# Kernel optimization log

Hardware: AMD Instinct MI355X
Metric: run time of the kernel (lower is better)

## Reference

```python
import jax, jax.numpy as jnp
import numpy as np


def setup_inputs() -> dict:
    key = jax.random.key(0)
    k1, k2, k3 = jax.random.split(key, 3)
    B, T, D = 32, 1024, 512
    x = jax.random.normal(k1, (B, T, D), dtype=jnp.float32)
    duration = jax.random.randint(k2, (B, T), 0, 9, dtype=jnp.int32)
    mask = jax.random.randint(k3, (B, T), 0, 2, dtype=jnp.int32)
    max_len = 2600  # static upper bound on max_b sum_t duration[b,t]
    return {"x": x, "duration": duration, "mask": mask, "max_len": max_len}


def reference(x, duration, mask, max_len):
    # x: [B, T, D]; duration, mask: [B, T]; max_len: python int (static)
    B, T, D = x.shape
    d_eff = duration * mask                       # masked tokens contribute 0 frames
    cum = jnp.cumsum(d_eff, axis=1)               # [B, T] cumulative frame counts
    total = cum[:, -1:]                           # [B, 1] frames per sequence
    pos = jnp.arange(max_len, dtype=cum.dtype)    # [T_out]
    # token index owning output frame j: #{t : cum[t] <= j}
    idx = jax.vmap(lambda c: jnp.searchsorted(c, pos, side='right'))(cum)  # [B, T_out]
    idx = jnp.minimum(idx, T - 1)
    valid = (pos[None, :] < total).astype(x.dtype)                         # [B, T_out]
    expanded = jnp.take_along_axis(x, idx[..., None], axis=1) * valid[..., None]
    return expanded, valid
```

## Files before the change

### kernel.cpp

```cpp
#include <hip/hip_runtime.h>

__global__ void lr_scan_kernel(const int* __restrict__ duration,
                               const int* __restrict__ mask,
                               int* __restrict__ cum, int T) {
    const int b = blockIdx.x;
    const int t = threadIdx.x;
    const int lane = t & 63;
    const int wave = t >> 6;
    __shared__ int wsum[4];

    const int4 dv = ((const int4*)(duration + (size_t)b * T))[t];
    const int4 mv = ((const int4*)(mask     + (size_t)b * T))[t];
    const int e0 = dv.x * mv.x, e1 = dv.y * mv.y,
              e2 = dv.z * mv.z, e3 = dv.w * mv.w;
    const int s3 = e0 + e1 + e2 + e3;

    int s = s3;
    #pragma unroll
    for (int off = 1; off < 64; off <<= 1) {
        int u = __shfl_up(s, off, 64);
        if (lane >= off) s += u;
    }
    if (lane == 63) wsum[wave] = s;
    __syncthreads();
    int bof = 0;
    #pragma unroll
    for (int w = 0; w < 4; ++w) bof += (w < wave) ? wsum[w] : 0;
    const int excl = bof + s - s3;

    int4 o;
    o.x = excl + e0;
    o.y = o.x + e1;
    o.z = o.y + e2;
    o.w = o.z + e3;
    ((int4*)(cum + (size_t)b * T))[t] = o;
}

__global__ __launch_bounds__(256)
void lr_fill_kernel(const int* __restrict__ cum,
                    int* __restrict__ idx,
                    float* __restrict__ valid_out,
                    int T, int max_len, int nwork) {
    const int gid = blockIdx.x * 256 + threadIdx.x;
    if (gid >= nwork) return;
    const unsigned b = (unsigned)gid / (unsigned)max_len;
    const int p = gid - (int)(b * (unsigned)max_len);

    const int* __restrict__ c = cum + (size_t)b * T;
    const int total = c[T - 1];
    if (p < total) {
        int lo = 0, hi = T;
        while (lo < hi) {
            int mid = (lo + hi) >> 1;
            if (c[mid] <= p) lo = mid + 1; else hi = mid;
        }
        idx[gid] = (lo < T - 1) ? lo : (T - 1);
        valid_out[gid] = 1.0f;
    } else {
        idx[gid] = -1;
        valid_out[gid] = 0.0f;
    }
}

__global__ __launch_bounds__(256)
void lr_copy_kernel(const float* __restrict__ x,
                    const int* __restrict__ idx,
                    float* __restrict__ out,
                    int T, int max_len, int nblk) {
    const int cpx = nblk >> 3;
    const int bid = blockIdx.x;
    const int swz = (bid & 7) * cpx + (bid >> 3);

    const int wave = threadIdx.x >> 6;
    const int lane = threadIdx.x & 63;
    const unsigned pos0 = (unsigned)swz * 8u + (unsigned)wave * 2u;
    const unsigned pos1 = pos0 + 1u;
    const unsigned b0 = pos0 / (unsigned)max_len;
    const unsigned b1 = pos1 / (unsigned)max_len;

    const int i0 = idx[pos0];
    const int i1 = idx[pos1];

    const float4 z = make_float4(0.f, 0.f, 0.f, 0.f);
    float4 a0 = z, a1 = z, c0 = z, c1 = z;
    if (i0 >= 0) {
        const float4* __restrict__ s0 =
            (const float4*)(x + ((size_t)b0 * T + i0) * 512u);
        a0 = s0[lane]; a1 = s0[lane + 64];
    }
    if (i1 >= 0) {
        const float4* __restrict__ s1 =
            (const float4*)(x + ((size_t)b1 * T + i1) * 512u);
        c0 = s1[lane]; c1 = s1[lane + 64];
    }
    float4* __restrict__ d0 = (float4*)(out + (size_t)pos0 * 512u);
    float4* __restrict__ d1 = (float4*)(out + (size_t)pos1 * 512u);
    d0[lane] = a0; d0[lane + 64] = a1;
    d1[lane] = c0; d1[lane + 64] = c1;
}

extern "C" void kernel_launch(void* const* d_in, const int* in_sizes, int n_in,
                              void* d_out, int out_size, void* d_ws, size_t ws_size,
                              hipStream_t stream) {
    const float* x        = (const float*)d_in[0];
    const int*   duration = (const int*)d_in[1];
    const int*   mask     = (const int*)d_in[2];

    const int B = 32;
    const int BT = in_sizes[1];
    const int T = BT / B;
    const int D = in_sizes[0] / BT;
    const int max_len = out_size / (B * (D + 1));

    float* out       = (float*)d_out;
    float* valid_out = out + (size_t)B * max_len * D;
    int*   cum       = (int*)d_ws;
    int*   idx       = cum + (size_t)B * T;

    lr_scan_kernel<<<B, 256, 0, stream>>>(duration, mask, cum, T);

    const int nwork = B * max_len;
    lr_fill_kernel<<<(nwork + 255) / 256, 256, 0, stream>>>(
        cum, idx, valid_out, T, max_len, nwork);

    const int nblk = nwork / 8;
    lr_copy_kernel<<<nblk, 256, 0, stream>>>(x, idx, out, T, max_len, nblk);
}
```

Baseline: 42.37 us.

## Fuse searchsorted into copy kernel with branchless search and nontemporal stores

Removes the separate fill kernel and the idx workspace. The copy kernel now does its own binary search over the cumulative counts, unrolled and branchless with power-of-two steps, and also writes the valid flags. Output stores become nontemporal. This saves a kernel launch and the idx round trip through memory. In exchange every wave repeats the search, and the fixed 512-step search assumes T is 1024.

New measurement: 42.67 us. No clear change (+0.7%).

```diff
diff --git a/kernel.cpp b/kernel.cpp
--- a/kernel.cpp
+++ b/kernel.cpp
@@ -1,4 +1,7 @@
 #include <hip/hip_runtime.h>
+
+typedef float f32x4 __attribute__((ext_vector_type(4)));
+typedef float f32x2 __attribute__((ext_vector_type(2)));
 
 __global__ void lr_scan_kernel(const int* __restrict__ duration,
                                const int* __restrict__ mask,
@@ -37,35 +40,10 @@
 }
 
 __global__ __launch_bounds__(256)
-void lr_fill_kernel(const int* __restrict__ cum,
-                    int* __restrict__ idx,
+void lr_copy_kernel(const float* __restrict__ x,
+                    const int* __restrict__ cum,
+                    float* __restrict__ out,
                     float* __restrict__ valid_out,
-                    int T, int max_len, int nwork) {
-    const int gid = blockIdx.x * 256 + threadIdx.x;
-    if (gid >= nwork) return;
-    const unsigned b = (unsigned)gid / (unsigned)max_len;
-    const int p = gid - (int)(b * (unsigned)max_len);
-
-    const int* __restrict__ c = cum + (size_t)b * T;
-    const int total = c[T - 1];
-    if (p < total) {
-        int lo = 0, hi = T;
-        while (lo < hi) {
-            int mid = (lo + hi) >> 1;
-            if (c[mid] <= p) lo = mid + 1; else hi = mid;
-        }
-        idx[gid] = (lo < T - 1) ? lo : (T - 1);
-        valid_out[gid] = 1.0f;
-    } else {
-        idx[gid] = -1;
-        valid_out[gid] = 0.0f;
-    }
-}
-
-__global__ __launch_bounds__(256)
-void lr_copy_kernel(const float* __restrict__ x,
-                    const int* __restrict__ idx,
-                    float* __restrict__ out,
                     int T, int max_len, int nblk) {
     const int cpx = nblk >> 3;
     const int bid = blockIdx.x;
@@ -77,26 +55,48 @@
     const unsigned pos1 = pos0 + 1u;
     const unsigned b0 = pos0 / (unsigned)max_len;
     const unsigned b1 = pos1 / (unsigned)max_len;
+    const int p0 = (int)(pos0 - b0 * (unsigned)max_len);
+    const int p1 = (int)(pos1 - b1 * (unsigned)max_len);
 
-    const int i0 = idx[pos0];
-    const int i1 = idx[pos1];
+    const int* __restrict__ c0 = cum + (size_t)b0 * T;
+    const int* __restrict__ c1 = cum + (size_t)b1 * T;
+    const int tot0 = c0[T - 1];
+    const int tot1 = c1[T - 1];
+    const bool v0 = p0 < tot0;
+    const bool v1 = p1 < tot1;
 
-    const float4 z = make_float4(0.f, 0.f, 0.f, 0.f);
-    float4 a0 = z, a1 = z, c0 = z, c1 = z;
-    if (i0 >= 0) {
-        const float4* __restrict__ s0 =
-            (const float4*)(x + ((size_t)b0 * T + i0) * 512u);
+    int r0 = 0, r1 = 0;
+    #pragma unroll
+    for (int step = 512; step >= 1; step >>= 1) {
+        if (c0[r0 + step - 1] <= p0) r0 += step;
+        if (c1[r1 + step - 1] <= p1) r1 += step;
+    }
+    const int i0 = (r0 < T - 1) ? r0 : (T - 1);
+    const int i1 = (r1 < T - 1) ? r1 : (T - 1);
+
+    const f32x4 z = {0.f, 0.f, 0.f, 0.f};
+    f32x4 a0 = z, a1 = z, cc0 = z, cc1 = z;
+    if (v0) {
+        const f32x4* __restrict__ s0 =
+            (const f32x4*)(x + ((size_t)b0 * T + i0) * 512u);
         a0 = s0[lane]; a1 = s0[lane + 64];
     }
-    if (i1 >= 0) {
-        const float4* __restrict__ s1 =
-            (const float4*)(x + ((size_t)b1 * T + i1) * 512u);
-        c0 = s1[lane]; c1 = s1[lane + 64];
+    if (v1) {
+        const f32x4* __restrict__ s1 =
+            (const f32x4*)(x + ((size_t)b1 * T + i1) * 512u);
+        cc0 = s1[lane]; cc1 = s1[lane + 64];
     }
-    float4* __restrict__ d0 = (float4*)(out + (size_t)pos0 * 512u);
-    float4* __restrict__ d1 = (float4*)(out + (size_t)pos1 * 512u);
-    d0[lane] = a0; d0[lane + 64] = a1;
-    d1[lane] = c0; d1[lane + 64] = c1;
+    f32x4* __restrict__ d0 = (f32x4*)(out + (size_t)pos0 * 512u);
+    f32x4* __restrict__ d1 = (f32x4*)(out + (size_t)pos1 * 512u);
+    __builtin_nontemporal_store(a0,  d0 + lane);
+    __builtin_nontemporal_store(a1,  d0 + lane + 64);
+    __builtin_nontemporal_store(cc0, d1 + lane);
+    __builtin_nontemporal_store(cc1, d1 + lane + 64);
+
+    if (lane == 0) {
+        f32x2 vv = {v0 ? 1.0f : 0.0f, v1 ? 1.0f : 0.0f};
+        __builtin_nontemporal_store(vv, (f32x2*)(valid_out + pos0));
+    }
 }
 
 extern "C" void kernel_launch(void* const* d_in, const int* in_sizes, int n_in,
@@ -115,14 +115,10 @@
     float* out       = (float*)d_out;
     float* valid_out = out + (size_t)B * max_len * D;
     int*   cum       = (int*)d_ws;
-    int*   idx       = cum + (size_t)B * T;
 
     lr_scan_kernel<<<B, 256, 0, stream>>>(duration, mask, cum, T);
 
-    const int nwork = B * max_len;
-    lr_fill_kernel<<<(nwork + 255) / 256, 256, 0, stream>>>(
-        cum, idx, valid_out, T, max_len, nwork);
-
-    const int nblk = nwork / 8;
-    lr_copy_kernel<<<nblk, 256, 0, stream>>>(x, idx, out, T, max_len, nblk);
+    const int nblk = (B * max_len) / 8;
+    lr_copy_kernel<<<nblk, 256, 0, stream>>>(x, cum, out, valid_out,
+                                             T, max_len, nblk);
 }
```
